# Optimization experiments

Hardware: AMD Instinct MI355X
Metric: run time of the kernel (lower is better)

The kernel has to match this reference:

```python
import jax, jax.numpy as jnp
import numpy as np

HIDDEN = 2048
N_HEADS = 16
N_KV_HEADS = 4
HEAD_DIM = HIDDEN // N_HEADS  # 128
BATCH = 1
SEQ = 2048
EPS = 1e-6


def _rms_norm(x, scale, eps=EPS):
    var = jnp.mean(jnp.square(x), axis=-1, keepdims=True)
    return x * jax.lax.rsqrt(var + eps) * scale


def _rotate_half(x):
    x1, x2 = jnp.split(x, 2, axis=-1)
    return jnp.concatenate((-x2, x1), axis=-1)


def setup_inputs() -> dict:
    key = jax.random.key(0)
    ks = jax.random.split(key, 8)
    hidden_states = jax.random.normal(ks[0], (BATCH, SEQ, HIDDEN), dtype=jnp.float32)
    # causal mask, broadcastable over [B, H, S, S]
    attention_mask = jnp.tril(jnp.ones((SEQ, SEQ), dtype=bool))[None, None, :, :]
    # standard RoPE tables, broadcastable against [B, S, H, D]
    inv_freq = 1.0 / (10000.0 ** (np.arange(0, HEAD_DIM, 2, dtype=np.float32) / HEAD_DIM))
    t = np.arange(SEQ, dtype=np.float32)
    freqs = np.outer(t, inv_freq)                      # [S, D/2]
    emb = np.concatenate([freqs, freqs], axis=-1)      # [S, D]
    cos = jnp.asarray(np.cos(emb))[:, None, :]         # [S, 1, D]
    sin = jnp.asarray(np.sin(emb))[:, None, :]
    s = 1.0 / np.sqrt(HIDDEN)
    Wq = jax.random.normal(ks[1], (HIDDEN, N_HEADS * HEAD_DIM), dtype=jnp.float32) * s
    Wk = jax.random.normal(ks[2], (HIDDEN, N_KV_HEADS * HEAD_DIM), dtype=jnp.float32) * s
    Wv = jax.random.normal(ks[3], (HIDDEN, N_KV_HEADS * HEAD_DIM), dtype=jnp.float32) * s
    Wo = jax.random.normal(ks[4], (HIDDEN, HIDDEN), dtype=jnp.float32) * s
    q_norm_scale = jnp.ones((HEAD_DIM,), dtype=jnp.float32)
    k_norm_scale = jnp.ones((HEAD_DIM,), dtype=jnp.float32)
    last_norm_scale = jnp.ones((HIDDEN,), dtype=jnp.float32)
    return {
        "hidden_states": hidden_states,
        "cos": cos,
        "sin": sin,
        "Wq": Wq,
        "Wk": Wk,
        "Wv": Wv,
        "Wo": Wo,
        "q_norm_scale": q_norm_scale,
        "k_norm_scale": k_norm_scale,
        "last_norm_scale": last_norm_scale,
        "attention_mask": attention_mask,
    }


def reference(hidden_states, cos, sin, Wq, Wk, Wv, Wo,
              q_norm_scale, k_norm_scale, last_norm_scale, attention_mask):
    B, S, _ = hidden_states.shape
    q = (hidden_states @ Wq).reshape(B, S, N_HEADS, HEAD_DIM)
    k = (hidden_states @ Wk).reshape(B, S, N_KV_HEADS, HEAD_DIM)
    v = (hidden_states @ Wv).reshape(B, S, N_KV_HEADS, HEAD_DIM)
    # per-head RMSNorm on Q/K
    q = _rms_norm(q, q_norm_scale)
    k = _rms_norm(k, k_norm_scale)
    # RoPE (cos/sin broadcast [S,1,D] -> [B,S,H,D])
    q = q * cos + _rotate_half(q) * sin
    k = k * cos + _rotate_half(k) * sin
    # GQA expansion
    groups = N_HEADS // N_KV_HEADS
    if groups > 1:
        k = jnp.repeat(k, groups, axis=2)
        v = jnp.repeat(v, groups, axis=2)
    out = jax.nn.dot_product_attention(q, k, v, mask=attention_mask)  # [B,S,H,D]
    out = out.reshape(B, S, HIDDEN) @ Wo
    return _rms_norm(out, last_norm_scale)
```

## Files before the change

### kernel.cpp

```cpp
#include <hip/hip_runtime.h>

typedef unsigned short u16;
typedef unsigned int u32;

#define S 2048
#define HID 2048
#define NH 16
#define NKV 4
#define D 128
#define QKVP 3072
#define QSCALE (0.08838834764831845f * 1.4426950408889634f)
#define NEG_INF -3.0e38f

typedef __attribute__((ext_vector_type(8))) short short8;
typedef __attribute__((ext_vector_type(4))) float f32x4;

__device__ __forceinline__ float bf2f(u16 u) {
  union { u32 i; float f; } c; c.i = ((u32)u) << 16; return c.f;
}
__device__ __forceinline__ u16 f2bf(float f) {
  union { float f; u32 i; } c; c.f = f;
  u32 x = c.i;
  u32 r = x + 0x7fffu + ((x >> 16) & 1u);
  return (u16)(r >> 16);
}

#if __has_builtin(__builtin_amdgcn_exp2f)
__device__ __forceinline__ float exp2_hw(float x) { return __builtin_amdgcn_exp2f(x); }
#else
__device__ __forceinline__ float exp2_hw(float x) { return exp2f(x); }
#endif

__device__ __forceinline__ u32 cvt_pk_bf16(float a, float b) {
  u32 r;
  asm("v_cvt_pk_bf16_f32 %0, %1, %2" : "=v"(r) : "v"(a), "v"(b));
  return r;
}

__device__ __forceinline__ void gload16(const u16* g, u16* l) {
  __builtin_amdgcn_global_load_lds(
      (const __attribute__((address_space(1))) u32*)g,
      (__attribute__((address_space(3))) u32*)l, 16, 0, 0);
}

__global__ __launch_bounds__(256) void k_cvt(const float* __restrict__ src,
                                             u16* __restrict__ dst) {
  int i = (blockIdx.x * 256 + threadIdx.x) * 8;
  float4 v0 = *(const float4*)(src + i);
  float4 v1 = *(const float4*)(src + i + 4);
  ushort4 w0, w1;
  w0.x = f2bf(v0.x); w0.y = f2bf(v0.y); w0.z = f2bf(v0.z); w0.w = f2bf(v0.w);
  w1.x = f2bf(v1.x); w1.y = f2bf(v1.y); w1.z = f2bf(v1.z); w1.w = f2bf(v1.w);
  *(ushort4*)(dst + i) = w0;
  *(ushort4*)(dst + i + 4) = w1;
}

__device__ __forceinline__ void transpose_body(const float* __restrict__ src,
                                               u16* __restrict__ dst,
                                               int N, int K, int nt, int kt,
                                               int t) {
  __shared__ float T[64][65];
#pragma unroll
  for (int it = 0; it < 4; ++it) {
    int r = it * 16 + (t >> 4), c = (t & 15) * 4;
    float4 v = *(const float4*)(src + (size_t)(kt + r) * N + nt + c);
    T[r][c] = v.x; T[r][c + 1] = v.y; T[r][c + 2] = v.z; T[r][c + 3] = v.w;
  }
  __syncthreads();
#pragma unroll
  for (int it = 0; it < 2; ++it) {
    int n = it * 32 + (t >> 3), k8 = (t & 7) * 8;
    ushort4 w0, w1;
    w0.x = f2bf(T[k8 + 0][n]); w0.y = f2bf(T[k8 + 1][n]);
    w0.z = f2bf(T[k8 + 2][n]); w0.w = f2bf(T[k8 + 3][n]);
    w1.x = f2bf(T[k8 + 4][n]); w1.y = f2bf(T[k8 + 5][n]);
    w1.z = f2bf(T[k8 + 6][n]); w1.w = f2bf(T[k8 + 7][n]);
    *(ushort4*)(dst + (size_t)(nt + n) * K + kt + k8) = w0;
    *(ushort4*)(dst + (size_t)(nt + n) * K + kt + k8 + 4) = w1;
  }
}

__global__ __launch_bounds__(256) void k_transpose(const float* __restrict__ src,
                                                   u16* __restrict__ dst,
                                                   int N, int K) {
  transpose_body(src, dst, N, K, blockIdx.x * 64, blockIdx.y * 64, threadIdx.x);
}

__global__ __launch_bounds__(256) void k_transpose_qkv(const float* __restrict__ Wq,
                                                       const float* __restrict__ Wk,
                                                       const float* __restrict__ Wv,
                                                       u16* __restrict__ WT) {
  const int bx = blockIdx.x;
  const float* src; u16* dst; int N, nt;
  if (bx < 32)      { src = Wq; dst = WT;                    N = 2048; nt = bx * 64; }
  else if (bx < 40) { src = Wk; dst = WT + 2048ull * 2048;   N = 512;  nt = (bx - 32) * 64; }
  else              { src = Wv; dst = WT + 2560ull * 2048;   N = 512;  nt = (bx - 40) * 64; }
  transpose_body(src, dst, N, 2048, nt, blockIdx.y * 64, threadIdx.x);
}

__global__ __launch_bounds__(256) void k_vt(const u16* __restrict__ QKV,
                                            u16* __restrict__ Vt) {
  __shared__ u16 T[64][66];
  const int t = threadIdx.x;
  const int s0 = blockIdx.x * 64, d0 = blockIdx.y * 64;
#pragma unroll
  for (int it = 0; it < 4; ++it) {
    int r = it * 16 + (t >> 4), c = (t & 15) * 4;
    ushort4 v = *(const ushort4*)(QKV + (size_t)(s0 + r) * QKVP + 2560 + d0 + c);
    T[r][c] = v.x; T[r][c + 1] = v.y; T[r][c + 2] = v.z; T[r][c + 3] = v.w;
  }
  __syncthreads();
#pragma unroll
  for (int it = 0; it < 4; ++it) {
    int dd = it * 16 + (t >> 4), sc = (t & 15) * 4;
    ushort4 w;
    w.x = T[sc + 0][dd]; w.y = T[sc + 1][dd];
    w.z = T[sc + 2][dd]; w.w = T[sc + 3][dd];
    *(ushort4*)(Vt + (size_t)(d0 + dd) * S + s0 + sc) = w;
  }
}

__global__ __launch_bounds__(256) void k_gemm_mfma(const u16* __restrict__ A,
                                                   const u16* __restrict__ BT,
                                                   void* __restrict__ Cout,
                                                   int N, int K, int out_bf16) {
  __shared__ __align__(16) u16 As[2][64 * 64];
  __shared__ __align__(16) u16 Bs[2][128 * 64];
  const int t = threadIdx.x, w = t >> 6, lane = t & 63;
  const int l15 = lane & 15, quad = lane >> 4;
  const int m0 = blockIdx.y * 64, n0 = blockIdx.x * 128;

  const int srow = lane >> 3;
  const int schunk = (lane & 7) ^ srow;
  const u16* Agb = A + (size_t)(m0 + w * 8 + srow) * K + schunk * 8;
  const u16* Bgb = BT + (size_t)(n0 + w * 8 + srow) * K + schunk * 8;

  f32x4 acc[4][2];
#pragma unroll
  for (int i = 0; i < 4; ++i)
#pragma unroll
    for (int j = 0; j < 2; ++j) acc[i][j] = (f32x4){0.f, 0.f, 0.f, 0.f};

  auto STAGE = [&](int k0, int b) {
#pragma unroll
    for (int it = 0; it < 2; ++it)
      gload16(Agb + (size_t)it * 32 * K + k0, &As[b][(w * 8 + it * 32) * 64]);
#pragma unroll
    for (int it = 0; it < 4; ++it)
      gload16(Bgb + (size_t)it * 32 * K + k0, &Bs[b][(w * 8 + it * 32) * 64]);
  };

  STAGE(0, 0);
  __syncthreads();
  int cur = 0;
  for (int k0 = 0; k0 < K; k0 += 64) {
    if (k0 + 64 < K) STAGE(k0 + 64, cur ^ 1);

    short8 af[4][2], bf[2][2];
#pragma unroll
    for (int k2 = 0; k2 < 2; ++k2) {
      int ch = (k2 * 4 + quad) ^ (l15 & 7);
#pragma unroll
      for (int i = 0; i < 4; ++i)
        af[i][k2] = *(const short8*)&As[cur][(i * 16 + l15) * 64 + ch * 8];
#pragma unroll
      for (int j = 0; j < 2; ++j)
        bf[j][k2] = *(const short8*)&Bs[cur][(w * 32 + j * 16 + l15) * 64 + ch * 8];
    }
#pragma unroll
    for (int k2 = 0; k2 < 2; ++k2)
#pragma unroll
      for (int i = 0; i < 4; ++i)
#pragma unroll
        for (int j = 0; j < 2; ++j)
          acc[i][j] = __builtin_amdgcn_mfma_f32_16x16x32_bf16(af[i][k2], bf[j][k2], acc[i][j], 0, 0, 0);

    __syncthreads();
    cur ^= 1;
  }

  if (out_bf16) {
    u16* C = (u16*)Cout;
#pragma unroll
    for (int i = 0; i < 4; ++i)
#pragma unroll
      for (int j = 0; j < 2; ++j) {
        int col = n0 + w * 32 + j * 16 + l15;
#pragma unroll
        for (int r = 0; r < 4; ++r)
          C[(size_t)(m0 + i * 16 + quad * 4 + r) * N + col] = f2bf(acc[i][j][r]);
      }
  } else {
    float* C = (float*)Cout;
#pragma unroll
    for (int i = 0; i < 4; ++i)
#pragma unroll
      for (int j = 0; j < 2; ++j) {
        int col = n0 + w * 32 + j * 16 + l15;
#pragma unroll
        for (int r = 0; r < 4; ++r)
          C[(size_t)(m0 + i * 16 + quad * 4 + r) * N + col] = acc[i][j][r];
      }
  }
}

__global__ __launch_bounds__(128) void k_norm_rope(u16* __restrict__ QKV,
                                                   const float* __restrict__ qsc,
                                                   const float* __restrict__ ksc,
                                                   const float* __restrict__ cosp,
                                                   const float* __restrict__ sinp) {
  const int s = blockIdx.x, hh = blockIdx.y, d = threadIdx.x;
  u16* row; const float* sc; float scale;
  if (hh < NH) { row = QKV + (size_t)s * QKVP + hh * D;            sc = qsc; scale = QSCALE; }
  else         { row = QKV + (size_t)s * QKVP + 2048 + (hh - NH) * D; sc = ksc; scale = 1.0f; }
  float x = bf2f(row[d]);
  float v = x * x;
#pragma unroll
  for (int o = 32; o; o >>= 1) v += __shfl_xor(v, o, 64);
  __shared__ float red[2];
  if ((d & 63) == 0) red[d >> 6] = v;
  __syncthreads();
  float var = (red[0] + red[1]) * (1.0f / 128.0f);
  float rinv = rsqrtf(var + 1e-6f) * scale;
  float xn = x * rinv * sc[d];
  __shared__ float sh[D];
  sh[d] = xn;
  __syncthreads();
  float rot = (d < 64) ? -sh[d + 64] : sh[d - 64];
  row[d] = f2bf(xn * cosp[s * D + d] + rot * sinp[s * D + d]);
}

#define KP 128
#define PTP 72

__global__ __launch_bounds__(256) void k_flash(const u16* __restrict__ QKV,
                                               const u16* __restrict__ Vt,
                                               u16* __restrict__ O) {
  const int h = blockIdx.y, g = h >> 2;
  const int qt = (h < 8) ? (31 - (int)blockIdx.x) : (int)blockIdx.x;
  const int t = threadIdx.x;
  const int w = t >> 6, lane = t & 63, l15 = lane & 15, quad = lane >> 4;

  __shared__ __align__(16) u16 Klds[2][64 * KP];
  __shared__ __align__(16) u16 Vlds[128 * 64];
  __shared__ __align__(16) u16 Pt[4][16 * PTP];

  const int qbase = qt * 64 + w * 16;
  const int qrow = qbase + l15;

  short8 qf[4];
  {
    const u16* qp = QKV + (size_t)qrow * QKVP + h * D + quad * 8;
#pragma unroll
    for (int c = 0; c < 4; ++c) qf[c] = *(const short8*)(qp + c * 32);
  }

  float m = NEG_INF, l = 0.f;
  f32x4 oacc[8];
#pragma unroll
  for (int nc = 0; nc < 8; ++nc) oacc[nc] = (f32x4){0.f, 0.f, 0.f, 0.f};

  const int nt = qt + 1;
  const int dd = t >> 3, cc = t & 7;

  auto KLOAD = [&](int j0, int b) {
#pragma unroll
    for (int it = 0; it < 4; ++it) {
      int rl = w * 16 + it * 4 + quad;
      int gchunk = (lane & 15) ^ (rl & 7);
      const u16* gp = QKV + (size_t)(j0 + rl) * QKVP + 2048 + g * D + gchunk * 8;
      gload16(gp, &Klds[b][(w * 16 + it * 4) * KP]);
    }
  };
  auto VLOAD = [&](int j0, uint4* vr) {
#pragma unroll
    for (int it = 0; it < 4; ++it)
      vr[it] = *(const uint4*)(Vt + (size_t)(g * D + dd + it * 32) * S + j0 + cc * 8);
  };
  auto VWRITE = [&](uint4* vr) {
#pragma unroll
    for (int it = 0; it < 4; ++it) {
      int d = dd + it * 32;
      *(uint4*)&Vlds[d * 64 + ((cc ^ (d & 7)) * 8)] = vr[it];
    }
  };
  auto COMPUTE = [&](int jt, int b) {
    const int j0 = jt * 64;
    f32x4 sa[4];
#pragma unroll
    for (int sub = 0; sub < 4; ++sub) {
      f32x4 acc = {0.f, 0.f, 0.f, 0.f};
#pragma unroll
      for (int c = 0; c < 4; ++c) {
        int ch = (c * 4 + quad) ^ (l15 & 7);
        short8 kf = *(const short8*)&Klds[b][(sub * 16 + l15) * KP + ch * 8];
        acc = __builtin_amdgcn_mfma_f32_16x16x32_bf16(kf, qf[c], acc, 0, 0, 0);
      }
      sa[sub] = acc;
    }
    if (jt == nt - 1) {
#pragma unroll
      for (int sub = 0; sub < 4; ++sub) {
        int keyb = j0 + sub * 16 + quad * 4;
#pragma unroll
        for (int r = 0; r < 4; ++r)
          if (keyb + r > qrow) sa[sub][r] = NEG_INF;
      }
    }
    float tmax = sa[0][0];
#pragma unroll
    for (int sub = 0; sub < 4; ++sub)
#pragma unroll
      for (int r = 0; r < 4; ++r) tmax = fmaxf(tmax, sa[sub][r]);
    tmax = fmaxf(tmax, __shfl_xor(tmax, 16, 64));
    tmax = fmaxf(tmax, __shfl_xor(tmax, 32, 64));
    float mn = fmaxf(m, tmax);
    float alpha = exp2_hw(m - mn);
    m = mn;
    float rs = 0.f;
#pragma unroll
    for (int sub = 0; sub < 4; ++sub) {
      float p0 = exp2_hw(sa[sub][0] - m);
      float p1 = exp2_hw(sa[sub][1] - m);
      float p2 = exp2_hw(sa[sub][2] - m);
      float p3 = exp2_hw(sa[sub][3] - m);
      rs += (p0 + p1) + (p2 + p3);
      u32 lo = cvt_pk_bf16(p0, p1);
      u32 hi = cvt_pk_bf16(p2, p3);
      *(uint2*)&Pt[w][l15 * PTP + sub * 16 + quad * 4] = make_uint2(lo, hi);
    }
    rs += __shfl_xor(rs, 16, 64);
    rs += __shfl_xor(rs, 32, 64);
    l = l * alpha + rs;
#pragma unroll
    for (int nc = 0; nc < 8; ++nc) {
      oacc[nc][0] *= alpha; oacc[nc][1] *= alpha;
      oacc[nc][2] *= alpha; oacc[nc][3] *= alpha;
    }
#pragma unroll
    for (int kc = 0; kc < 2; ++kc) {
      short8 pf = *(const short8*)&Pt[w][l15 * PTP + kc * 32 + quad * 8];
#pragma unroll
      for (int nc = 0; nc < 8; ++nc) {
        int d = nc * 16 + l15;
        short8 vf = *(const short8*)&Vlds[d * 64 + (((kc * 4 + quad) ^ (d & 7)) * 8)];
        oacc[nc] = __builtin_amdgcn_mfma_f32_16x16x32_bf16(vf, pf, oacc[nc], 0, 0, 0);
      }
    }
  };

  uint4 vrA[4], vrB[4];
  KLOAD(0, 0);
  VLOAD(0, vrA);
  for (int jt = 0; jt < nt; jt += 2) {
    __syncthreads();
    VWRITE(vrA);
    __syncthreads();
    if (jt + 1 < nt) { KLOAD((jt + 1) * 64, 1); VLOAD((jt + 1) * 64, vrB); }
    COMPUTE(jt, 0);
    if (jt + 1 < nt) {
      __syncthreads();
      VWRITE(vrB);
      __syncthreads();
      if (jt + 2 < nt) { KLOAD((jt + 2) * 64, 0); VLOAD((jt + 2) * 64, vrA); }
      COMPUTE(jt + 1, 1);
    }
  }

  float inv = 1.0f / l;
  u16* orow = O + (size_t)qrow * HID + h * D;
#pragma unroll
  for (int nc = 0; nc < 8; ++nc) {
    ushort4 wv;
    wv.x = f2bf(oacc[nc][0] * inv); wv.y = f2bf(oacc[nc][1] * inv);
    wv.z = f2bf(oacc[nc][2] * inv); wv.w = f2bf(oacc[nc][3] * inv);
    *(ushort4*)(orow + nc * 16 + quad * 4) = wv;
  }
}

__device__ __forceinline__ float blockSum256(float v, float* red, int t) {
#pragma unroll
  for (int o = 32; o; o >>= 1) v += __shfl_xor(v, o, 64);
  if ((t & 63) == 0) red[t >> 6] = v;
  __syncthreads();
  v = red[0] + red[1] + red[2] + red[3];
  __syncthreads();
  return v;
}

__global__ __launch_bounds__(256) void k_fnorm(const float* __restrict__ X,
                                               const float* __restrict__ sc,
                                               float* __restrict__ out) {
  const int s = blockIdx.x, t = threadIdx.x;
  const float* row = X + (size_t)s * HID;
  float4 r0 = *(const float4*)(row + t * 8);
  float4 r1 = *(const float4*)(row + t * 8 + 4);
  float x[8] = {r0.x, r0.y, r0.z, r0.w, r1.x, r1.y, r1.z, r1.w};
  float ss = 0.f;
#pragma unroll
  for (int ii = 0; ii < 8; ++ii) ss += x[ii] * x[ii];
  __shared__ float red[4];
  float tot = blockSum256(ss, red, t);
  float rinv = rsqrtf(tot * (1.0f / 2048.0f) + 1e-6f);
  float4 s0 = *(const float4*)(sc + t * 8);
  float4 s1 = *(const float4*)(sc + t * 8 + 4);
  float4 w0 = make_float4(x[0] * rinv * s0.x, x[1] * rinv * s0.y,
                          x[2] * rinv * s0.z, x[3] * rinv * s0.w);
  float4 w1 = make_float4(x[4] * rinv * s1.x, x[5] * rinv * s1.y,
                          x[6] * rinv * s1.z, x[7] * rinv * s1.w);
  *(float4*)(out + (size_t)s * HID + t * 8) = w0;
  *(float4*)(out + (size_t)s * HID + t * 8 + 4) = w1;
}

extern "C" void kernel_launch(void* const* d_in, const int* in_sizes, int n_in,
                              void* d_out, int out_size, void* d_ws, size_t ws_size,
                              hipStream_t stream) {
  const float* hidden = (const float*)d_in[0];
  const float* cosp   = (const float*)d_in[1];
  const float* sinp   = (const float*)d_in[2];
  const float* Wq     = (const float*)d_in[3];
  const float* Wk     = (const float*)d_in[4];
  const float* Wv     = (const float*)d_in[5];
  const float* Wo     = (const float*)d_in[6];
  const float* qsc    = (const float*)d_in[7];
  const float* ksc    = (const float*)d_in[8];
  const float* lsc    = (const float*)d_in[9];
  float* out = (float*)d_out;

  char* ws = (char*)d_ws;
  u16*   Hb  = (u16*)(ws);
  u16*   WoT = (u16*)(ws);
  u16*   WT  = (u16*)(ws + (8ull << 20));
  u16*   An  = (u16*)(ws + (8ull << 20));
  u16*   QKV = (u16*)(ws + (20ull << 20));
  float* Ob  = (float*)(ws + (20ull << 20));
  u16*   Vtb = (u16*)(ws + (32ull << 20));

  k_cvt<<<S * HID / (256 * 8), 256, 0, stream>>>(hidden, Hb);
  k_transpose_qkv<<<dim3(48, 32), 256, 0, stream>>>(Wq, Wk, Wv, WT);
  k_gemm_mfma<<<dim3(24, 32), 256, 0, stream>>>(Hb, WT, QKV, QKVP, 2048, 1);
  k_transpose<<<dim3(32, 32), 256, 0, stream>>>(Wo, WoT, 2048, 2048);
  k_norm_rope<<<dim3(S, NH + NKV), 128, 0, stream>>>(QKV, qsc, ksc, cosp, sinp);
  k_vt<<<dim3(32, 8), 256, 0, stream>>>(QKV, Vtb);
  k_flash<<<dim3(32, NH), 256, 0, stream>>>(QKV, Vtb, An);
  k_gemm_mfma<<<dim3(16, 32), 256, 0, stream>>>(An, WoT, Ob, 2048, 2048, 0);
  k_fnorm<<<S, 256, 0, stream>>>(Ob, lsc, out);
}
```

Baseline: 295.9 us.

## Merge prep kernels, vectorize norm-rope per wave, hoist QK^T before loads

Folds the hidden-state bf16 conversion and the QKV weight transpose into a single launch, which removes one kernel launch. The norm+RoPE kernel now handles one head per wavefront with two elements per lane. It swaps the shared-memory reductions and barriers for wave shuffles and uses packed loads and stores. In flash attention, the QK^T MFMAs are issued before the next tile's K/V global loads so they can overlap, at the cost of restructuring the compute lambda.

Measured after the change: 285.4 us. 1.04x faster.

```diff
diff --git a/kernel.cpp b/kernel.cpp
--- a/kernel.cpp
+++ b/kernel.cpp
@@ -41,18 +41,6 @@
   __builtin_amdgcn_global_load_lds(
       (const __attribute__((address_space(1))) u32*)g,
       (__attribute__((address_space(3))) u32*)l, 16, 0, 0);
-}
-
-__global__ __launch_bounds__(256) void k_cvt(const float* __restrict__ src,
-                                             u16* __restrict__ dst) {
-  int i = (blockIdx.x * 256 + threadIdx.x) * 8;
-  float4 v0 = *(const float4*)(src + i);
-  float4 v1 = *(const float4*)(src + i + 4);
-  ushort4 w0, w1;
-  w0.x = f2bf(v0.x); w0.y = f2bf(v0.y); w0.z = f2bf(v0.z); w0.w = f2bf(v0.w);
-  w1.x = f2bf(v1.x); w1.y = f2bf(v1.y); w1.z = f2bf(v1.z); w1.w = f2bf(v1.w);
-  *(ushort4*)(dst + i) = w0;
-  *(ushort4*)(dst + i + 4) = w1;
 }
 
 __device__ __forceinline__ void transpose_body(const float* __restrict__ src,
@@ -80,22 +68,37 @@
   }
 }
 
+__global__ __launch_bounds__(256) void k_pre(const float* __restrict__ hidden,
+                                             u16* __restrict__ Hb,
+                                             const float* __restrict__ Wq,
+                                             const float* __restrict__ Wk,
+                                             const float* __restrict__ Wv,
+                                             u16* __restrict__ WT) {
+  const int bx = blockIdx.x, t = threadIdx.x;
+  if (bx < 2048) {
+    int i = (bx * 256 + t) * 8;
+    float4 v0 = *(const float4*)(hidden + i);
+    float4 v1 = *(const float4*)(hidden + i + 4);
+    ushort4 w0, w1;
+    w0.x = f2bf(v0.x); w0.y = f2bf(v0.y); w0.z = f2bf(v0.z); w0.w = f2bf(v0.w);
+    w1.x = f2bf(v1.x); w1.y = f2bf(v1.y); w1.z = f2bf(v1.z); w1.w = f2bf(v1.w);
+    *(ushort4*)(Hb + i) = w0;
+    *(ushort4*)(Hb + i + 4) = w1;
+    return;
+  }
+  const int id = bx - 2048;
+  const int x = id % 48, y = id / 48;
+  const float* src; u16* dst; int N, nt;
+  if (x < 32)      { src = Wq; dst = WT;                    N = 2048; nt = x * 64; }
+  else if (x < 40) { src = Wk; dst = WT + 2048ull * 2048;   N = 512;  nt = (x - 32) * 64; }
+  else             { src = Wv; dst = WT + 2560ull * 2048;   N = 512;  nt = (x - 40) * 64; }
+  transpose_body(src, dst, N, 2048, nt, y * 64, t);
+}
+
 __global__ __launch_bounds__(256) void k_transpose(const float* __restrict__ src,
                                                    u16* __restrict__ dst,
                                                    int N, int K) {
   transpose_body(src, dst, N, K, blockIdx.x * 64, blockIdx.y * 64, threadIdx.x);
-}
-
-__global__ __launch_bounds__(256) void k_transpose_qkv(const float* __restrict__ Wq,
-                                                       const float* __restrict__ Wk,
-                                                       const float* __restrict__ Wv,
-                                                       u16* __restrict__ WT) {
-  const int bx = blockIdx.x;
-  const float* src; u16* dst; int N, nt;
-  if (bx < 32)      { src = Wq; dst = WT;                    N = 2048; nt = bx * 64; }
-  else if (bx < 40) { src = Wk; dst = WT + 2048ull * 2048;   N = 512;  nt = (bx - 32) * 64; }
-  else              { src = Wv; dst = WT + 2560ull * 2048;   N = 512;  nt = (bx - 40) * 64; }
-  transpose_body(src, dst, N, 2048, nt, blockIdx.y * 64, threadIdx.x);
 }
 
 __global__ __launch_bounds__(256) void k_vt(const u16* __restrict__ QKV,
@@ -204,30 +207,33 @@
   }
 }
 
-__global__ __launch_bounds__(128) void k_norm_rope(u16* __restrict__ QKV,
+__global__ __launch_bounds__(256) void k_norm_rope(u16* __restrict__ QKV,
                                                    const float* __restrict__ qsc,
                                                    const float* __restrict__ ksc,
                                                    const float* __restrict__ cosp,
                                                    const float* __restrict__ sinp) {
-  const int s = blockIdx.x, hh = blockIdx.y, d = threadIdx.x;
+  const int s = blockIdx.x;
+  const int w = threadIdx.x >> 6, lane = threadIdx.x & 63;
+  const int hh = blockIdx.y * 4 + w;
   u16* row; const float* sc; float scale;
-  if (hh < NH) { row = QKV + (size_t)s * QKVP + hh * D;            sc = qsc; scale = QSCALE; }
+  if (hh < NH) { row = QKV + (size_t)s * QKVP + hh * D;               sc = qsc; scale = QSCALE; }
   else         { row = QKV + (size_t)s * QKVP + 2048 + (hh - NH) * D; sc = ksc; scale = 1.0f; }
-  float x = bf2f(row[d]);
-  float v = x * x;
+  const int d0 = lane * 2;
+  u32 pr = *(const u32*)(row + d0);
+  float x0 = bf2f((u16)(pr & 0xffffu)), x1 = bf2f((u16)(pr >> 16));
+  float v = x0 * x0 + x1 * x1;
 #pragma unroll
   for (int o = 32; o; o >>= 1) v += __shfl_xor(v, o, 64);
-  __shared__ float red[2];
-  if ((d & 63) == 0) red[d >> 6] = v;
-  __syncthreads();
-  float var = (red[0] + red[1]) * (1.0f / 128.0f);
-  float rinv = rsqrtf(var + 1e-6f) * scale;
-  float xn = x * rinv * sc[d];
-  __shared__ float sh[D];
-  sh[d] = xn;
-  __syncthreads();
-  float rot = (d < 64) ? -sh[d + 64] : sh[d - 64];
-  row[d] = f2bf(xn * cosp[s * D + d] + rot * sinp[s * D + d]);
+  float rinv = rsqrtf(v * (1.0f / 128.0f) + 1e-6f) * scale;
+  float xn0 = x0 * rinv * sc[d0], xn1 = x1 * rinv * sc[d0 + 1];
+  float p0 = __shfl_xor(xn0, 32, 64);
+  float p1 = __shfl_xor(xn1, 32, 64);
+  float sgn = (lane < 32) ? -1.f : 1.f;
+  float2 c  = *(const float2*)(cosp + (size_t)s * D + d0);
+  float2 sn = *(const float2*)(sinp + (size_t)s * D + d0);
+  float o0 = xn0 * c.x + sgn * p0 * sn.x;
+  float o1 = xn1 * c.y + sgn * p1 * sn.y;
+  *(u32*)(row + d0) = cvt_pk_bf16(o0, o1);
 }
 
 #define KP 128
@@ -284,9 +290,7 @@
       *(uint4*)&Vlds[d * 64 + ((cc ^ (d & 7)) * 8)] = vr[it];
     }
   };
-  auto COMPUTE = [&](int jt, int b) {
-    const int j0 = jt * 64;
-    f32x4 sa[4];
+  auto QKT = [&](int b, f32x4* sa) {
 #pragma unroll
     for (int sub = 0; sub < 4; ++sub) {
       f32x4 acc = {0.f, 0.f, 0.f, 0.f};
@@ -298,6 +302,9 @@
       }
       sa[sub] = acc;
     }
+  };
+  auto SMPV = [&](int jt, f32x4* sa) {
+    const int j0 = jt * 64;
     if (jt == nt - 1) {
 #pragma unroll
       for (int sub = 0; sub < 4; ++sub) {
@@ -350,20 +357,23 @@
   };
 
   uint4 vrA[4], vrB[4];
+  f32x4 sa[4];
   KLOAD(0, 0);
   VLOAD(0, vrA);
   for (int jt = 0; jt < nt; jt += 2) {
     __syncthreads();
     VWRITE(vrA);
     __syncthreads();
+    QKT(0, sa);
     if (jt + 1 < nt) { KLOAD((jt + 1) * 64, 1); VLOAD((jt + 1) * 64, vrB); }
-    COMPUTE(jt, 0);
+    SMPV(jt, sa);
     if (jt + 1 < nt) {
       __syncthreads();
       VWRITE(vrB);
       __syncthreads();
+      QKT(1, sa);
       if (jt + 2 < nt) { KLOAD((jt + 2) * 64, 0); VLOAD((jt + 2) * 64, vrA); }
-      COMPUTE(jt + 1, 1);
+      SMPV(jt + 1, sa);
     }
   }
 
@@ -436,11 +446,10 @@
   float* Ob  = (float*)(ws + (20ull << 20));
   u16*   Vtb = (u16*)(ws + (32ull << 20));
 
-  k_cvt<<<S * HID / (256 * 8), 256, 0, stream>>>(hidden, Hb);
-  k_transpose_qkv<<<dim3(48, 32), 256, 0, stream>>>(Wq, Wk, Wv, WT);
+  k_pre<<<2048 + 1536, 256, 0, stream>>>(hidden, Hb, Wq, Wk, Wv, WT);
   k_gemm_mfma<<<dim3(24, 32), 256, 0, stream>>>(Hb, WT, QKV, QKVP, 2048, 1);
   k_transpose<<<dim3(32, 32), 256, 0, stream>>>(Wo, WoT, 2048, 2048);
-  k_norm_rope<<<dim3(S, NH + NKV), 128, 0, stream>>>(QKV, qsc, ksc, cosp, sinp);
+  k_norm_rope<<<dim3(S, 5), 256, 0, stream>>>(QKV, qsc, ksc, cosp, sinp);
   k_vt<<<dim3(32, 8), 256, 0, stream>>>(QKV, Vtb);
   k_flash<<<dim3(32, NH), 256, 0, stream>>>(QKV, Vtb, An);
   k_gemm_mfma<<<dim3(16, 32), 256, 0, stream>>>(An, WoT, Ob, 2048, 2048, 0);
```
